# Performance work log

Measured on AMD Instinct MI355X. Metric: run time of the kernel, lower is better.

The kernel has to match this reference:

```python
import jax, jax.numpy as jnp
import numpy as np

T, NB, NCLASS, L = 256, 64, 7357, 50


def setup_inputs() -> dict:
    key = jax.random.key(0)
    k1, k2 = jax.random.split(key)
    dense_pred = jax.random.normal(k1, (T, NB, NCLASS), dtype=jnp.float32)
    target = jax.random.randint(k2, (NB, L), 0, NCLASS, dtype=jnp.int64)
    return {"dense_pred": dense_pred, "target": target}


def reference(dense_pred, target):
    # dense_pred: [T, nB, nClass], target: [nB, L] int labels, 0 = stop/blank
    nB, Llen = target.shape
    nClass = dense_pred.shape[-1]
    dense_prob = jax.nn.softmax(dense_pred, axis=2)  # [T, nB, nClass]

    # The torch loop zeroes hollow_param[tt[j]] for j until the FIRST 0 in the
    # target sequence (break). valid[b, j] == 1 iff target[b, :j+1] are all nonzero.
    valid = jnp.cumprod((target != 0).astype(jnp.int32), axis=1)  # [nB, L]
    # Invalid positions map to class 0, which is zeroed unconditionally anyway.
    eff_idx = jnp.where(valid == 1, target, 0)  # [nB, L]

    hollow = jnp.ones((nB, nClass), dtype=dense_pred.dtype)
    hollow = hollow.at[:, 0].set(0.0)
    rows = jnp.broadcast_to(jnp.arange(nB)[:, None], (nB, Llen))
    hollow = hollow.at[rows, eff_idx].set(0.0)  # scatter zeros at target classes

    prob_sum = dense_prob.sum(0)  # [nB, nClass]
    whace_loss = (prob_sum * hollow).mean()
    return whace_loss
```

## Files before the change

kernel.cpp:

```cpp
#include <hip/hip_runtime.h>
#include <math.h>

#define TT 256
#define NB 64
#define NC 7357
#define LL 50
#define NROWS (TT * NB)
#define NBLK 2048
#define ROWS_PER_WAVE 2

typedef float f32x4 __attribute__((ext_vector_type(4)));

__global__ void prep_kernel(const int* __restrict__ target,
                            int* __restrict__ nz, int* __restrict__ cls) {
    int b = threadIdx.x;
    if (b >= NB) return;
    int list[LL + 1];
    int n = 0;
    list[n++] = 0;
    for (int j = 0; j < LL; ++j) {
        int t = target[b * LL + j];
        if (t == 0) break;
        bool found = false;
        for (int k = 0; k < n; ++k) {
            if (list[k] == t) { found = true; break; }
        }
        if (!found) list[n++] = t;
    }
    nz[b] = n;
    for (int k = 0; k < n; ++k) cls[b * 64 + k] = list[k];
}

__device__ __forceinline__ float fexp(float v) { return __expf(v); }

__global__ __launch_bounds__(256, 4) void row_kernel(const float* __restrict__ x,
                                                     const int* __restrict__ nz,
                                                     const int* __restrict__ cls,
                                                     float* __restrict__ partial) {
    const int lane = threadIdx.x & 63;
    const int gwave = (blockIdx.x << 2) | (threadIdx.x >> 6);

#pragma unroll
    for (int r = 0; r < ROWS_PER_WAVE; ++r) {
        const int row = gwave * ROWS_PER_WAVE + r;
        const int b = row & (NB - 1);
        const float* rp = x + (size_t)row * NC;

        const int peel = (4 - (row & 3)) & 3;
        const int rem = NC - peel;
        const int nvec = rem >> 2;
        const int tail = rem & 3;
        const f32x4* vp = (const f32x4*)(rp + peel);

        const int n = nz[b];
        float xg = (lane < n) ? rp[cls[b * 64 + lane]] : -INFINITY;

        float ex1 = (lane < peel) ? rp[lane] : -INFINITY;
        float ex2 = (lane < tail) ? rp[peel + (nvec << 2) + lane] : -INFINITY;

        float s = fexp(ex1) + fexp(ex2);

        int i = lane;
#pragma unroll
        for (int c = 0; c < 7; ++c) {
            f32x4 q0 = __builtin_nontemporal_load(vp + i);
            f32x4 q1 = __builtin_nontemporal_load(vp + i + 64);
            f32x4 q2 = __builtin_nontemporal_load(vp + i + 128);
            f32x4 q3 = __builtin_nontemporal_load(vp + i + 192);
            s += fexp(q0.x) + fexp(q0.y) + fexp(q0.z) + fexp(q0.w);
            s += fexp(q1.x) + fexp(q1.y) + fexp(q1.z) + fexp(q1.w);
            s += fexp(q2.x) + fexp(q2.y) + fexp(q2.z) + fexp(q2.w);
            s += fexp(q3.x) + fexp(q3.y) + fexp(q3.z) + fexp(q3.w);
            i += 256;
        }
        if (i < nvec) {
            f32x4 q = __builtin_nontemporal_load(vp + i);
            s += fexp(q.x) + fexp(q.y) + fexp(q.z) + fexp(q.w);
        }

        float z = fexp(xg);

        for (int o = 32; o > 0; o >>= 1) {
            s += __shfl_down(s, o);
            z += __shfl_down(z, o);
        }
        if (lane == 0) partial[row] = 1.0f - z / s;
    }
}

__global__ __launch_bounds__(256) void final_kernel(const float* __restrict__ partial,
                                                    float* __restrict__ out) {
    const f32x4* p4 = (const f32x4*)partial;
    float s = 0.0f;
    int i = threadIdx.x;
#pragma unroll
    for (int c = 0; c < 16; ++c) {
        f32x4 q = p4[i];
        s += q.x + q.y + q.z + q.w;
        i += 256;
    }
    for (int o = 32; o > 0; o >>= 1) s += __shfl_down(s, o);
    __shared__ float sr[4];
    if ((threadIdx.x & 63) == 0) sr[threadIdx.x >> 6] = s;
    __syncthreads();
    if (threadIdx.x == 0)
        out[0] = (sr[0] + sr[1] + sr[2] + sr[3]) * (1.0f / ((float)NB * (float)NC));
}

extern "C" void kernel_launch(void* const* d_in, const int* in_sizes, int n_in,
                              void* d_out, int out_size, void* d_ws, size_t ws_size,
                              hipStream_t stream) {
    const float* dense_pred = (const float*)d_in[0];
    const int* target = (const int*)d_in[1];
    float* out = (float*)d_out;

    int* nz = (int*)d_ws;
    int* cls = nz + 64;
    float* partial = (float*)(cls + 64 * 64);

    prep_kernel<<<1, 64, 0, stream>>>(target, nz, cls);
    row_kernel<<<NBLK, 256, 0, stream>>>(dense_pred, nz, cls, partial);
    final_kernel<<<1, 256, 0, stream>>>(partial, out);
}
```

Measured before the change: 189.9 us.

## Stream input in flat 256-float windows and reassemble per-row exp sums

New measurement: 208.4 us. 1.1x slower.

```diff
diff --git a/kernel.cpp b/kernel.cpp
--- a/kernel.cpp
+++ b/kernel.cpp
@@ -6,8 +6,9 @@
 #define NC 7357
 #define LL 50
 #define NROWS (TT * NB)
+#define NFLOAT (NROWS * NC)
+#define NWIN (NFLOAT / 256)
 #define NBLK 2048
-#define ROWS_PER_WAVE 2
 
 typedef float f32x4 __attribute__((ext_vector_type(4)));
 
@@ -22,9 +23,8 @@
         int t = target[b * LL + j];
         if (t == 0) break;
         bool found = false;
-        for (int k = 0; k < n; ++k) {
+        for (int k = 0; k < n; ++k)
             if (list[k] == t) { found = true; break; }
-        }
         if (!found) list[n++] = t;
     }
     nz[b] = n;
@@ -32,6 +32,96 @@
 }
 
 __device__ __forceinline__ float fexp(float v) { return __expf(v); }
+
+__global__ __launch_bounds__(256, 4) void stream_kernel(const float* __restrict__ x,
+                                                        float2* __restrict__ win) {
+    const int lane = threadIdx.x & 63;
+    const int gwave = (blockIdx.x << 2) | (threadIdx.x >> 6);
+    const f32x4* vp = (const f32x4*)x;
+
+    for (int u = gwave; u < NWIN; u += 8192) {
+        f32x4 q = __builtin_nontemporal_load(vp + ((size_t)u * 64 + lane));
+        float e0 = fexp(q.x), e1 = fexp(q.y), e2 = fexp(q.z), e3 = fexp(q.w);
+
+        const int fbase = u << 8;
+        const int r1 = fbase / NC;
+        const int r2 = (fbase + 255) / NC;
+        float sA, sB;
+        if (r1 == r2) {
+            sA = (e0 + e1) + (e2 + e3);
+            for (int o = 32; o > 0; o >>= 1) sA += __shfl_down(sA, o);
+            sB = 0.0f;
+        } else {
+            const int B = r2 * NC;
+            const int f0 = fbase + (lane << 2);
+            sA = 0.0f; sB = 0.0f;
+            if (f0 + 0 < B) sA += e0; else sB += e0;
+            if (f0 + 1 < B) sA += e1; else sB += e1;
+            if (f0 + 2 < B) sA += e2; else sB += e2;
+            if (f0 + 3 < B) sA += e3; else sB += e3;
+            for (int o = 32; o > 0; o >>= 1) {
+                sA += __shfl_down(sA, o);
+                sB += __shfl_down(sB, o);
+            }
+        }
+        if (lane == 0) win[u] = make_float2(sA, sB);
+    }
+}
+
+__global__ __launch_bounds__(256) void row2_kernel(const float* __restrict__ x,
+                                                   const float2* __restrict__ win,
+                                                   const int* __restrict__ nz,
+                                                   const int* __restrict__ cls,
+                                                   float* __restrict__ partial) {
+    const int lane = threadIdx.x & 63;
+    const int wave = threadIdx.x >> 6;
+    const int row = (blockIdx.x << 2) | wave;
+    const int b = row & (NB - 1);
+
+    const int f0 = row * NC;
+    const int u0 = f0 >> 8;
+    const int u1 = (f0 + NC - 1) >> 8;
+
+    float S = 0.0f;
+    const int u = u0 + lane;
+    if (u <= u1) {
+        float2 w = win[u];
+        const int fb = u << 8;
+        const int r1 = fb / NC;
+        const int r2 = (fb + 255) / NC;
+        if (r1 == row) S += w.x;
+        if (r2 == row && r1 != row) S += w.y;
+    }
+
+    const int n = nz[b];
+    float z = 0.0f;
+    if (lane < n) z = fexp(x[(size_t)f0 + cls[b * 64 + lane]]);
+
+    for (int o = 32; o > 0; o >>= 1) {
+        S += __shfl_down(S, o);
+        z += __shfl_down(z, o);
+    }
+    if (lane == 0) partial[row] = 1.0f - z / S;
+}
+
+__global__ __launch_bounds__(256) void final_kernel(const float* __restrict__ partial,
+                                                    float* __restrict__ out) {
+    const f32x4* p4 = (const f32x4*)partial;
+    float s = 0.0f;
+    int i = threadIdx.x;
+#pragma unroll
+    for (int c = 0; c < 16; ++c) {
+        f32x4 q = p4[i];
+        s += q.x + q.y + q.z + q.w;
+        i += 256;
+    }
+    for (int o = 32; o > 0; o >>= 1) s += __shfl_down(s, o);
+    __shared__ float sr[4];
+    if ((threadIdx.x & 63) == 0) sr[threadIdx.x >> 6] = s;
+    __syncthreads();
+    if (threadIdx.x == 0)
+        out[0] = (sr[0] + sr[1] + sr[2] + sr[3]) * (1.0f / ((float)NB * (float)NC));
+}
 
 __global__ __launch_bounds__(256, 4) void row_kernel(const float* __restrict__ x,
                                                      const int* __restrict__ nz,
@@ -41,11 +131,10 @@
     const int gwave = (blockIdx.x << 2) | (threadIdx.x >> 6);
 
 #pragma unroll
-    for (int r = 0; r < ROWS_PER_WAVE; ++r) {
-        const int row = gwave * ROWS_PER_WAVE + r;
+    for (int r = 0; r < 2; ++r) {
+        const int row = gwave * 2 + r;
         const int b = row & (NB - 1);
         const float* rp = x + (size_t)row * NC;
-
         const int peel = (4 - (row & 3)) & 3;
         const int rem = NC - peel;
         const int nvec = rem >> 2;
@@ -54,10 +143,8 @@
 
         const int n = nz[b];
         float xg = (lane < n) ? rp[cls[b * 64 + lane]] : -INFINITY;
-
         float ex1 = (lane < peel) ? rp[lane] : -INFINITY;
         float ex2 = (lane < tail) ? rp[peel + (nvec << 2) + lane] : -INFINITY;
-
         float s = fexp(ex1) + fexp(ex2);
 
         int i = lane;
@@ -77,34 +164,13 @@
             f32x4 q = __builtin_nontemporal_load(vp + i);
             s += fexp(q.x) + fexp(q.y) + fexp(q.z) + fexp(q.w);
         }
-
         float z = fexp(xg);
-
         for (int o = 32; o > 0; o >>= 1) {
             s += __shfl_down(s, o);
             z += __shfl_down(z, o);
         }
         if (lane == 0) partial[row] = 1.0f - z / s;
     }
-}
-
-__global__ __launch_bounds__(256) void final_kernel(const float* __restrict__ partial,
-                                                    float* __restrict__ out) {
-    const f32x4* p4 = (const f32x4*)partial;
-    float s = 0.0f;
-    int i = threadIdx.x;
-#pragma unroll
-    for (int c = 0; c < 16; ++c) {
-        f32x4 q = p4[i];
-        s += q.x + q.y + q.z + q.w;
-        i += 256;
-    }
-    for (int o = 32; o > 0; o >>= 1) s += __shfl_down(s, o);
-    __shared__ float sr[4];
-    if ((threadIdx.x & 63) == 0) sr[threadIdx.x >> 6] = s;
-    __syncthreads();
-    if (threadIdx.x == 0)
-        out[0] = (sr[0] + sr[1] + sr[2] + sr[3]) * (1.0f / ((float)NB * (float)NC));
 }
 
 extern "C" void kernel_launch(void* const* d_in, const int* in_sizes, int n_in,
@@ -114,11 +180,25 @@
     const int* target = (const int*)d_in[1];
     float* out = (float*)d_out;
 
-    int* nz = (int*)d_ws;
+    char* ws = (char*)d_ws;
+    float2* win = (float2*)ws;
+    int* nz = (int*)(ws + (size_t)NWIN * 8);
     int* cls = nz + 64;
-    float* partial = (float*)(cls + 64 * 64);
-
-    prep_kernel<<<1, 64, 0, stream>>>(target, nz, cls);
-    row_kernel<<<NBLK, 256, 0, stream>>>(dense_pred, nz, cls, partial);
-    final_kernel<<<1, 256, 0, stream>>>(partial, out);
-}
+    float* partial = (float*)(ws + (size_t)NWIN * 8 + 256 + 64 * 64 * 4);
+
+    const size_t need = (size_t)NWIN * 8 + 256 + 64 * 64 * 4 + NROWS * 4;
+
+    if (ws_size >= need) {
+        prep_kernel<<<1, 64, 0, stream>>>(target, nz, cls);
+        stream_kernel<<<NBLK, 256, 0, stream>>>(dense_pred, win);
+        row2_kernel<<<NROWS / 4, 256, 0, stream>>>(dense_pred, win, nz, cls, partial);
+        final_kernel<<<1, 256, 0, stream>>>(partial, out);
+    } else {
+        int* nz2 = (int*)d_ws;
+        int* cls2 = nz2 + 64;
+        float* partial2 = (float*)(cls2 + 64 * 64);
+        prep_kernel<<<1, 64, 0, stream>>>(target, nz2, cls2);
+        row_kernel<<<NBLK, 256, 0, stream>>>(dense_pred, nz2, cls2, partial2);
+        final_kernel<<<1, 256, 0, stream>>>(partial2, out);
+    }
+}
```
